# Kernel tuning notes

Measured on AMD Instinct MI355X. Metric: run time of the kernel, lower is better.

Reference implementation:

```python
import jax, jax.numpy as jnp
import numpy as np

B, L, C, R = 8192, 49, 512, 128  # L = 7*7 hardcoded in module
H = W = 7


def _conv2d(x, w, b, pad):
    # x: (B, Cin, H, W), w: (Cout, Cin, k, k)
    y = jax.lax.conv_general_dilated(
        x, w, window_strides=(1, 1), padding=[(pad, pad), (pad, pad)],
        dimension_numbers=("NCHW", "OIHW", "NCHW"))
    return y + b[None, :, None, None]


def _star_relu(x, scale, bias):
    r = jnp.maximum(x, 0.0)
    return scale * (r * r) + bias


def setup_inputs() -> dict:
    key = jax.random.key(0)
    ks = jax.random.split(key, 12)
    s = 0.05
    return {
        "x": jax.random.normal(ks[0], (B, L, C), jnp.float32),
        "g_reduce_w": jax.random.normal(ks[1], (R, C), jnp.float32) * s,
        "l_reduce_w": jax.random.normal(ks[2], (R, C), jnp.float32) * s,
        "conv3_w": jax.random.normal(ks[3], (R // 2, R // 2, 3, 3), jnp.float32) * s,
        "conv3_b": jax.random.normal(ks[4], (R // 2,), jnp.float32) * s,
        "conv5_w": jax.random.normal(ks[5], (R - R // 2, R - R // 2, 5, 5), jnp.float32) * s,
        "conv5_b": jax.random.normal(ks[6], (R - R // 2,), jnp.float32) * s,
        "channel_w": jax.random.normal(ks[7], (C, R), jnp.float32) * s,
        "channel_b": jax.random.normal(ks[8], (C,), jnp.float32) * s,
        "spatial_w": jax.random.normal(ks[9], (1, 3 * R), jnp.float32) * s,
        "spatial_b": jax.random.normal(ks[10], (1,), jnp.float32) * s,
        "star_scale": jnp.ones((1,), jnp.float32),
        "star_bias": jnp.zeros((1,), jnp.float32),
    }


def reference(x, g_reduce_w, l_reduce_w, conv3_w, conv3_b, conv5_w, conv5_b,
              channel_w, channel_b, spatial_w, spatial_b, star_scale, star_bias):
    # x: (B, L, C) with L = 49 (7x7)
    # Global dual pooling over spatial (== over L)
    x_max = jnp.max(x, axis=1)   # (B, C)
    x_avg = jnp.mean(x, axis=1)  # (B, C)
    # g_reduce 1x1 conv (no bias) + StarReLU
    g1 = _star_relu(x_max @ g_reduce_w.T, star_scale, star_bias)  # (B, R)
    g2 = _star_relu(x_avg @ g_reduce_w.T, star_scale, star_bias)  # (B, R)
    # Local branch: 1x1 reduce -> HybConv2d (split 3x3 / 5x5) -> StarReLU
    x_img = x.transpose(0, 2, 1).reshape(B, C, H, W)
    x_l = jnp.einsum("bchw,rc->brhw", x_img, l_reduce_w)  # (B, R, 7, 7)
    xl1, xl2 = x_l[:, :R // 2], x_l[:, R // 2:]
    y1 = _conv2d(xl1, conv3_w, conv3_b, pad=1)
    y2 = _conv2d(xl2, conv5_w, conv5_b, pad=2)
    x_l = _star_relu(jnp.concatenate([y1, y2], axis=1), star_scale, star_bias)
    x_l = x_l.reshape(B, R, L).transpose(0, 2, 1)  # (B, L, R)
    # Channel gate: Linear(R->C) applied to each pooled branch, summed
    c_aggr = jax.nn.sigmoid((g1 @ channel_w.T + channel_b)
                            + (g2 @ channel_w.T + channel_b))  # (B, C)
    # Spatial gate: concat [x_l, g1 broadcast, g2 broadcast] -> Linear(3R->1)
    g1b = jnp.broadcast_to(g1[:, None, :], (B, L, R))
    g2b = jnp.broadcast_to(g2[:, None, :], (B, L, R))
    s_cat = jnp.concatenate([x_l, g1b, g2b], axis=-1)  # (B, L, 3R)
    s_aggr = jax.nn.sigmoid(jnp.einsum("blk,ok->blo", s_cat, spatial_w) + spatial_b)  # (B, L, 1)
    aggr = c_aggr[:, None, :] * s_aggr  # (B, L, C)
    return x * aggr
```

## Files before the change

kernel.cpp:

```cpp
#include <hip/hip_runtime.h>
#include <math.h>

#define B_ 8192
#define L_ 49
#define C_ 512
#define R_ 128

typedef short   bf16x8 __attribute__((ext_vector_type(8)));
typedef unsigned short u16x8 __attribute__((ext_vector_type(8)));
typedef float   f32x4  __attribute__((ext_vector_type(4)));

#define WS_LWF   0
#define WS_WB3F  65536
#define WS_WB5F  102400
#define WS_GWF   204800
#define WS_CWF   270336

#define SM_G     0
#define SM_CA    1024
#define SM_SPW   3072
#define SM_SP    5120
#define SM_GDOT  5376
#define SM_XB    0
#define SM_XLB   50176
#define SM_MAXB  50176
#define SM_SUMF  54272
#define SM_GA    62976
#define SM_TOT   65024

__device__ __forceinline__ float bf2f(unsigned short u) {
    union { float f; unsigned int i; } v; v.i = ((unsigned int)u) << 16; return v.f;
}
__device__ __forceinline__ unsigned short f2bf(float f) {
    union { float f; unsigned int i; } v; v.f = f;
    unsigned int r = v.i + 0x7fffu + ((v.i >> 16) & 1u);
    return (unsigned short)(r >> 16);
}
__device__ __forceinline__ float star_relu(float x, float sc, float bi) {
    float r = fmaxf(x, 0.f);
    return sc * r * r + bi;
}
__device__ __forceinline__ float sigmoidf_(float x) {
    return 1.f / (1.f + __expf(-x));
}

__global__ void cvt_weights(const float* __restrict__ lw, const float* __restrict__ w3,
                            const float* __restrict__ w5, const float* __restrict__ gw,
                            const float* __restrict__ cw, unsigned short* __restrict__ ws)
{
    int t = blockIdx.x * blockDim.x + threadIdx.x;
    int stride = gridDim.x * blockDim.x;
    for (int i = t; i < 65536; i += stride) {
        int j = i & 7, lane = (i >> 3) & 63, ks = (i >> 9) & 15, nt = i >> 13;
        int n = nt * 16 + (lane & 15);
        int k = ks * 32 + (lane >> 4) * 8 + j;
        ws[WS_LWF + i] = f2bf(lw[n * 512 + k]);
        ws[WS_GWF + i] = f2bf(gw[n * 512 + k]);
    }
    for (int i = t; i < 65536; i += stride) {
        int j = i & 7, c = (i >> 3) & 511, r8 = i >> 12;
        ws[WS_CWF + i] = f2bf(cw[c * 128 + r8 * 8 + j]);
    }
    for (int i = t; i < 36864; i += stride) {
        int j = i & 7, lane = (i >> 3) & 63, ks = (i >> 9) & 1, f = (i >> 10) & 3, tap = i >> 12;
        int oc = f * 16 + (lane & 15);
        int ic = ks * 32 + (lane >> 4) * 8 + j;
        ws[WS_WB3F + i] = f2bf(w3[(oc * 64 + ic) * 9 + tap]);
    }
    for (int i = t; i < 102400; i += stride) {
        int j = i & 7, lane = (i >> 3) & 63, ks = (i >> 9) & 1, f = (i >> 10) & 3, tap = i >> 12;
        int oc = f * 16 + (lane & 15);
        int ic = ks * 32 + (lane >> 4) * 8 + j;
        ws[WS_WB5F + i] = f2bf(w5[(oc * 64 + ic) * 25 + tap]);
    }
}

template <int NTAP, int KD, int PAD, int COLBASE>
__device__ __forceinline__ void conv_mfma(const unsigned short* __restrict__ s_xlb,
                                          const unsigned short* __restrict__ wtbf,
                                          int m16, int kg, int ln, int f, f32x4 C[4])
{
    int lp_[4], i_[4], j_[4];
    #pragma unroll
    for (int mf = 0; mf < 4; ++mf) {
        lp_[mf] = mf * 16 + m16;
        i_[mf] = lp_[mf] / 7;
        j_[mf] = lp_[mf] % 7;
    }
    bf16x8 cur0 = *(const bf16x8*)(wtbf + ((0 * 4 + f) * 2 + 0) * 512 + ln * 8);
    bf16x8 cur1 = *(const bf16x8*)(wtbf + ((0 * 4 + f) * 2 + 1) * 512 + ln * 8);
    #pragma unroll
    for (int tap = 0; tap < NTAP; ++tap) {
        bf16x8 nxt0 = cur0, nxt1 = cur1;
        if (tap + 1 < NTAP) {
            nxt0 = *(const bf16x8*)(wtbf + (((tap + 1) * 4 + f) * 2 + 0) * 512 + ln * 8);
            nxt1 = *(const bf16x8*)(wtbf + (((tap + 1) * 4 + f) * 2 + 1) * 512 + ln * 8);
        }
        const int dy = tap / KD - PAD, dx = tap % KD - PAD;
        int lc[4];
        #pragma unroll
        for (int mf = 0; mf < 4; ++mf) {
            int ii = i_[mf] + dy, jj = j_[mf] + dx;
            bool v = (lp_[mf] < 49) & (ii >= 0) & (ii < 7) & (jj >= 0) & (jj < 7);
            lc[mf] = v ? (ii * 7 + jj) : 49;
        }
        #pragma unroll
        for (int mf = 0; mf < 4; ++mf) {
            int chunk0 = ((COLBASE >> 3) + kg) ^ (lc[mf] & 7);
            bf16x8 a = *(const bf16x8*)&s_xlb[lc[mf] * 128 + chunk0 * 8];
            C[mf] = __builtin_amdgcn_mfma_f32_16x16x32_bf16(a, cur0, C[mf], 0, 0, 0);
        }
        #pragma unroll
        for (int mf = 0; mf < 4; ++mf) {
            int chunk1 = ((COLBASE >> 3) + 4 + kg) ^ (lc[mf] & 7);
            bf16x8 a = *(const bf16x8*)&s_xlb[lc[mf] * 128 + chunk1 * 8];
            C[mf] = __builtin_amdgcn_mfma_f32_16x16x32_bf16(a, cur1, C[mf], 0, 0, 0);
        }
        cur0 = nxt0; cur1 = nxt1;
    }
}

__global__ __launch_bounds__(512, 4)
void mafn_fused(const float* __restrict__ x,
                const float* __restrict__ b3, const float* __restrict__ b5,
                const float* __restrict__ cb, const float* __restrict__ sw,
                const float* __restrict__ sb, const float* __restrict__ ssc,
                const float* __restrict__ sbi,
                const unsigned short* __restrict__ ws,
                float* __restrict__ out)
{
    __shared__ __align__(16) unsigned char smem[SM_TOT];
    unsigned short* s_xb   = (unsigned short*)(smem + SM_XB);
    unsigned short* s_xlb  = (unsigned short*)(smem + SM_XLB);
    unsigned short* s_maxb = (unsigned short*)(smem + SM_MAXB);
    float*          s_sumf = (float*)(smem + SM_SUMF);
    unsigned short* s_ga   = (unsigned short*)(smem + SM_GA);
    float*          s_g    = (float*)(smem + SM_G);
    float*          s_ca   = (float*)(smem + SM_CA);
    float*          s_spw  = (float*)(smem + SM_SPW);
    float*          s_sp   = (float*)(smem + SM_SP);
    float*          s_gdot = (float*)(smem + SM_GDOT);

    const int b = blockIdx.x, t = threadIdx.x;
    const int wv = t >> 6, ln = t & 63;
    const int m16 = ln & 15, kg = ln >> 4;
    const float scale = ssc[0], sbias = sbi[0];

    const unsigned short* lwf  = ws + WS_LWF;
    const unsigned short* wb3f = ws + WS_WB3F;
    const unsigned short* wb5f = ws + WS_WB5F;
    const unsigned short* gwf  = ws + WS_GWF;
    const unsigned short* cwf  = ws + WS_CWF;

    f32x4 accA[4];
    f32x4 accG;
    {
        const f32x4 z = {0.f, 0.f, 0.f, 0.f};
        #pragma unroll
        for (int mf = 0; mf < 4; ++mf) accA[mf] = z;
        accG = z;
    }

    {
        const float4* x4 = (const float4*)(x + (size_t)b * (L_ * C_));
        const int c4 = t & 127, rg = t >> 7;
        const int l0 = rg * 12;
        const int nl = (rg < 3) ? 12 : 13;
        float4 mx = {-3.4e38f, -3.4e38f, -3.4e38f, -3.4e38f};
        float4 sm = {0.f, 0.f, 0.f, 0.f};
        for (int li = 0; li < nl; ++li) {
            int l = l0 + li;
            float4 v = x4[l * 128 + c4];
            mx.x = fmaxf(mx.x, v.x); mx.y = fmaxf(mx.y, v.y);
            mx.z = fmaxf(mx.z, v.z); mx.w = fmaxf(mx.w, v.w);
            sm.x += v.x; sm.y += v.y; sm.z += v.z; sm.w += v.w;
            ushort4 p;
            p.x = f2bf(v.x); p.y = f2bf(v.y); p.z = f2bf(v.z); p.w = f2bf(v.w);
            int chunk = (c4 >> 1) ^ (l & 7);
            *(ushort4*)&s_xb[l * 512 + chunk * 8 + (c4 & 1) * 4] = p;
        }
        ushort4 pm;
        pm.x = f2bf(mx.x); pm.y = f2bf(mx.y); pm.z = f2bf(mx.z); pm.w = f2bf(mx.w);
        *(ushort4*)&s_maxb[rg * 512 + c4 * 4] = pm;
        *(float4*)&s_sumf[rg * 512 + c4 * 4] = sm;
    }
    __syncthreads();

    {
        int c = t;
        float m = bf2f(s_maxb[c]);
        #pragma unroll
        for (int i = 1; i < 4; ++i) m = fmaxf(m, bf2f(s_maxb[i * 512 + c]));
        float s = 0.f;
        #pragma unroll
        for (int i = 0; i < 4; ++i) s += s_sumf[i * 512 + c];
        s_ga[c] = f2bf(m);
        s_ga[512 + c] = f2bf(s * (1.f / 49.f));
    }
    __syncthreads();

    {
        int rowA[4];
        #pragma unroll
        for (int mf = 0; mf < 4; ++mf) rowA[mf] = min(mf * 16 + m16, 48);

        bf16x8 bb0 = *(const bf16x8*)(lwf + (wv * 16 + 0) * 512 + ln * 8);
        bf16x8 bb1 = *(const bf16x8*)(lwf + (wv * 16 + 1) * 512 + ln * 8);
        #pragma unroll
        for (int ks = 0; ks < 16; ++ks) {
            bf16x8 bn = bb1;
            if (ks + 2 < 16)
                bn = *(const bf16x8*)(lwf + (wv * 16 + ks + 2) * 512 + ln * 8);
            #pragma unroll
            for (int mf = 0; mf < 4; ++mf) {
                int chunk = (ks * 4 + kg) ^ (rowA[mf] & 7);
                bf16x8 a = *(const bf16x8*)&s_xb[rowA[mf] * 512 + chunk * 8];
                accA[mf] = __builtin_amdgcn_mfma_f32_16x16x32_bf16(a, bb0, accA[mf], 0, 0, 0);
            }
            bb0 = bb1; bb1 = bn;
        }

        bf16x8 gb0 = *(const bf16x8*)(gwf + (wv * 16 + 0) * 512 + ln * 8);
        bf16x8 gb1 = *(const bf16x8*)(gwf + (wv * 16 + 1) * 512 + ln * 8);
        const bf16x8 zz = {0,0,0,0,0,0,0,0};
        #pragma unroll
        for (int ks = 0; ks < 16; ++ks) {
            bf16x8 gn = gb1;
            if (ks + 2 < 16)
                gn = *(const bf16x8*)(gwf + (wv * 16 + ks + 2) * 512 + ln * 8);
            bf16x8 a = (m16 < 2) ? *(const bf16x8*)&s_ga[m16 * 512 + ks * 32 + kg * 8] : zz;
            accG = __builtin_amdgcn_mfma_f32_16x16x32_bf16(a, gb0, accG, 0, 0, 0);
            gb0 = gb1; gb1 = gn;
        }
    }
    __syncthreads();

    {
        if (t < 64) ((unsigned int*)(s_xlb + 49 * 128))[t] = 0;
        const int n = wv * 16 + m16;
        #pragma unroll
        for (int mf = 0; mf < 4; ++mf) {
            #pragma unroll
            for (int rg = 0; rg < 4; ++rg) {
                int lp = mf * 16 + kg * 4 + rg;
                if (lp < 49) {
                    int idx = lp * 128 + ((((n >> 3) ^ (lp & 7)) << 3) + (n & 7));
                    s_xlb[idx] = f2bf(accA[mf][rg]);
                }
            }
        }
        if (kg == 0) {
            s_g[n]       = star_relu(accG[0], scale, sbias);
            s_g[128 + n] = star_relu(accG[1], scale, sbias);
        }
    }
    __syncthreads();

    const int f_ = wv & 3;
    const int oc_ = f_ * 16 + m16;
    {
        f32x4 C[4];
        const f32x4 z = {0.f, 0.f, 0.f, 0.f};
        #pragma unroll
        for (int mf = 0; mf < 4; ++mf) C[mf] = z;

        if (wv < 4) {
            conv_mfma<25, 5, 2, 64>(s_xlb, wb5f, m16, kg, ln, f_, C);
        } else {
            conv_mfma< 9, 3, 1,  0>(s_xlb, wb3f, m16, kg, ln, f_, C);
            const int idx = t - 256;
            #pragma unroll
            for (int half = 0; half < 2; ++half) {
                int c = idx + half * 256;
                float a0 = 0.f, a1 = 0.f;
                #pragma unroll 4
                for (int r8 = 0; r8 < 16; ++r8) {
                    u16x8 w = *(const u16x8*)(cwf + r8 * 4096 + c * 8);
                    float p = 0.f;
                    #pragma unroll
                    for (int k = 0; k < 8; ++k)
                        p += bf2f(w[k]) * (s_g[r8 * 8 + k] + s_g[128 + r8 * 8 + k]);
                    if (r8 & 1) a1 += p; else a0 += p;
                }
                s_ca[c] = sigmoidf_(a0 + a1 + 2.f * cb[c]);
            }
            if (wv == 7) {
                float p = s_g[ln] * sw[128 + ln] + s_g[128 + ln] * sw[256 + ln]
                        + s_g[ln + 64] * sw[128 + ln + 64] + s_g[128 + ln + 64] * sw[256 + ln + 64];
                #pragma unroll
                for (int off = 32; off > 0; off >>= 1) p += __shfl_xor(p, off);
                if (ln == 0) s_gdot[0] = p;
            }
        }

        const bool is5 = (wv < 4);
        const int ch = is5 ? 64 + oc_ : oc_;
        const float bias = is5 ? b5[oc_] : b3[oc_];
        const float sww = sw[ch];
        #pragma unroll
        for (int mf = 0; mf < 4; ++mf) {
            #pragma unroll
            for (int rg = 0; rg < 4; ++rg) {
                int lp = mf * 16 + kg * 4 + rg;
                float v = (lp < 49) ? star_relu(C[mf][rg] + bias, scale, sbias) * sww : 0.f;
                v += __shfl_xor(v, 1);
                v += __shfl_xor(v, 2);
                v += __shfl_xor(v, 4);
                v += __shfl_xor(v, 8);
                if (m16 == 0 && lp < 49) s_spw[wv * 64 + lp] = v;
            }
        }
    }
    __syncthreads();

    if (t < 49) {
        float s = s_gdot[0] + sb[0];
        #pragma unroll
        for (int w = 0; w < 8; ++w) s += s_spw[w * 64 + t];
        s_sp[t] = sigmoidf_(s);
    }
    __syncthreads();

    {
        const float4* x4 = (const float4*)(x + (size_t)b * (L_ * C_));
        float4* o4 = (float4*)(out + (size_t)b * (L_ * C_));
        const int c4 = t & 127;
        const float4 cv = *(const float4*)&s_ca[c4 * 4];
        for (int i = t; i < 49 * 128; i += 512) {
            int l = i >> 7;
            float4 xv = x4[i];
            float g = s_sp[l];
            float4 ov;
            ov.x = xv.x * cv.x * g;
            ov.y = xv.y * cv.y * g;
            ov.z = xv.z * cv.z * g;
            ov.w = xv.w * cv.w * g;
            o4[i] = ov;
        }
    }
}

extern "C" void kernel_launch(void* const* d_in, const int* in_sizes, int n_in,
                              void* d_out, int out_size, void* d_ws, size_t ws_size,
                              hipStream_t stream) {
    (void)in_sizes; (void)n_in; (void)ws_size; (void)out_size;
    const float* x    = (const float*)d_in[0];
    const float* g_w  = (const float*)d_in[1];
    const float* l_w  = (const float*)d_in[2];
    const float* w3   = (const float*)d_in[3];
    const float* b3   = (const float*)d_in[4];
    const float* w5   = (const float*)d_in[5];
    const float* b5   = (const float*)d_in[6];
    const float* cw   = (const float*)d_in[7];
    const float* cb   = (const float*)d_in[8];
    const float* sw   = (const float*)d_in[9];
    const float* sb   = (const float*)d_in[10];
    const float* ssc  = (const float*)d_in[11];
    const float* sbi  = (const float*)d_in[12];
    float* outp = (float*)d_out;
    unsigned short* ws = (unsigned short*)d_ws;

    cvt_weights<<<dim3(512), dim3(256), 0, stream>>>(l_w, w3, w5, g_w, cw, ws);
    mafn_fused<<<dim3(B_), dim3(512), 0, stream>>>(
        x, b3, b5, cb, sw, sb, ssc, sbi, ws, outp);
}
```

Measured before the change: 602.2 us.

## Drop fourth conv MFMA row tile and compute last pixel with scalar FMAs

The conv MFMA loop now covers only three 16-row tiles (pixels 0-47). Pixel 48 is computed separately on the 3x3 waves with scalar FP32 dot products over raw weights, then reduced by shuffles and an LDS atomic. The goal is to cut about a quarter of conv MFMA work and A-fragment LDS reads. Bf16 packing also moves to the v_cvt_pk_bf16_f32 instruction. In exchange, the 3x3 waves carry extra scalar work and uncoalesced global weight reads, which may lengthen the critical path.

```diff
diff --git a/kernel.cpp b/kernel.cpp
--- a/kernel.cpp
+++ b/kernel.cpp
@@ -35,6 +35,11 @@
     union { float f; unsigned int i; } v; v.f = f;
     unsigned int r = v.i + 0x7fffu + ((v.i >> 16) & 1u);
     return (unsigned short)(r >> 16);
+}
+__device__ __forceinline__ unsigned int pkbf(float a, float b) {
+    unsigned int r;
+    asm("v_cvt_pk_bf16_f32 %0, %1, %2" : "=v"(r) : "v"(a), "v"(b));
+    return r;
 }
 __device__ __forceinline__ float star_relu(float x, float sc, float bi) {
     float r = fmaxf(x, 0.f);
@@ -78,11 +83,11 @@
 template <int NTAP, int KD, int PAD, int COLBASE>
 __device__ __forceinline__ void conv_mfma(const unsigned short* __restrict__ s_xlb,
                                           const unsigned short* __restrict__ wtbf,
-                                          int m16, int kg, int ln, int f, f32x4 C[4])
+                                          int m16, int kg, int ln, int f, f32x4 C[3])
 {
-    int lp_[4], i_[4], j_[4];
+    int lp_[3], i_[3], j_[3];
     #pragma unroll
-    for (int mf = 0; mf < 4; ++mf) {
+    for (int mf = 0; mf < 3; ++mf) {
         lp_[mf] = mf * 16 + m16;
         i_[mf] = lp_[mf] / 7;
         j_[mf] = lp_[mf] % 7;
@@ -97,21 +102,21 @@
             nxt1 = *(const bf16x8*)(wtbf + (((tap + 1) * 4 + f) * 2 + 1) * 512 + ln * 8);
         }
         const int dy = tap / KD - PAD, dx = tap % KD - PAD;
-        int lc[4];
-        #pragma unroll
-        for (int mf = 0; mf < 4; ++mf) {
+        int lc[3];
+        #pragma unroll
+        for (int mf = 0; mf < 3; ++mf) {
             int ii = i_[mf] + dy, jj = j_[mf] + dx;
-            bool v = (lp_[mf] < 49) & (ii >= 0) & (ii < 7) & (jj >= 0) & (jj < 7);
+            bool v = (ii >= 0) & (ii < 7) & (jj >= 0) & (jj < 7);
             lc[mf] = v ? (ii * 7 + jj) : 49;
         }
         #pragma unroll
-        for (int mf = 0; mf < 4; ++mf) {
+        for (int mf = 0; mf < 3; ++mf) {
             int chunk0 = ((COLBASE >> 3) + kg) ^ (lc[mf] & 7);
             bf16x8 a = *(const bf16x8*)&s_xlb[lc[mf] * 128 + chunk0 * 8];
             C[mf] = __builtin_amdgcn_mfma_f32_16x16x32_bf16(a, cur0, C[mf], 0, 0, 0);
         }
         #pragma unroll
-        for (int mf = 0; mf < 4; ++mf) {
+        for (int mf = 0; mf < 3; ++mf) {
             int chunk1 = ((COLBASE >> 3) + 4 + kg) ^ (lc[mf] & 7);
             bf16x8 a = *(const bf16x8*)&s_xlb[lc[mf] * 128 + chunk1 * 8];
             C[mf] = __builtin_amdgcn_mfma_f32_16x16x32_bf16(a, cur1, C[mf], 0, 0, 0);
@@ -126,6 +131,7 @@
                 const float* __restrict__ cb, const float* __restrict__ sw,
                 const float* __restrict__ sb, const float* __restrict__ ssc,
                 const float* __restrict__ sbi,
+                const float* __restrict__ w3raw, const float* __restrict__ w5raw,
                 const unsigned short* __restrict__ ws,
                 float* __restrict__ out)
 {
@@ -174,14 +180,12 @@
             mx.x = fmaxf(mx.x, v.x); mx.y = fmaxf(mx.y, v.y);
             mx.z = fmaxf(mx.z, v.z); mx.w = fmaxf(mx.w, v.w);
             sm.x += v.x; sm.y += v.y; sm.z += v.z; sm.w += v.w;
-            ushort4 p;
-            p.x = f2bf(v.x); p.y = f2bf(v.y); p.z = f2bf(v.z); p.w = f2bf(v.w);
+            uint2 p; p.x = pkbf(v.x, v.y); p.y = pkbf(v.z, v.w);
             int chunk = (c4 >> 1) ^ (l & 7);
-            *(ushort4*)&s_xb[l * 512 + chunk * 8 + (c4 & 1) * 4] = p;
-        }
-        ushort4 pm;
-        pm.x = f2bf(mx.x); pm.y = f2bf(mx.y); pm.z = f2bf(mx.z); pm.w = f2bf(mx.w);
-        *(ushort4*)&s_maxb[rg * 512 + c4 * 4] = pm;
+            *(uint2*)&s_xb[l * 512 + chunk * 8 + (c4 & 1) * 4] = p;
+        }
+        uint2 pm; pm.x = pkbf(mx.x, mx.y); pm.y = pkbf(mx.z, mx.w);
+        *(uint2*)&s_maxb[rg * 512 + c4 * 4] = pm;
         *(float4*)&s_sumf[rg * 512 + c4 * 4] = sm;
     }
     __syncthreads();
@@ -237,15 +241,22 @@
 
     {
         if (t < 64) ((unsigned int*)(s_xlb + 49 * 128))[t] = 0;
+        if (t < 8)  s_spw[t * 64 + 48] = 0.f;
+        if (t == 8) s_gdot[1] = 0.f;
         const int n = wv * 16 + m16;
         #pragma unroll
         for (int mf = 0; mf < 4; ++mf) {
             #pragma unroll
-            for (int rg = 0; rg < 4; ++rg) {
-                int lp = mf * 16 + kg * 4 + rg;
-                if (lp < 49) {
-                    int idx = lp * 128 + ((((n >> 3) ^ (lp & 7)) << 3) + (n & 7));
-                    s_xlb[idx] = f2bf(accA[mf][rg]);
+            for (int rp = 0; rp < 2; ++rp) {
+                unsigned int u = pkbf(accA[mf][rp * 2], accA[mf][rp * 2 + 1]);
+                int lp0 = mf * 16 + kg * 4 + rp * 2;
+                if (lp0 < 49) {
+                    int idx = lp0 * 128 + ((((n >> 3) ^ (lp0 & 7)) << 3) + (n & 7));
+                    s_xlb[idx] = (unsigned short)u;
+                }
+                if (lp0 + 1 < 49) {
+                    int idx = (lp0 + 1) * 128 + ((((n >> 3) ^ ((lp0 + 1) & 7)) << 3) + (n & 7));
+                    s_xlb[idx] = (unsigned short)(u >> 16);
                 }
             }
         }
@@ -259,10 +270,10 @@
     const int f_ = wv & 3;
     const int oc_ = f_ * 16 + m16;
     {
-        f32x4 C[4];
+        f32x4 C[3];
         const f32x4 z = {0.f, 0.f, 0.f, 0.f};
         #pragma unroll
-        for (int mf = 0; mf < 4; ++mf) C[mf] = z;
+        for (int mf = 0; mf < 3; ++mf) C[mf] = z;
 
         if (wv < 4) {
             conv_mfma<25, 5, 2, 64>(s_xlb, wb5f, m16, kg, ln, f_, C);
@@ -284,6 +295,40 @@
                 }
                 s_ca[c] = sigmoidf_(a0 + a1 + 2.f * cb[c]);
             }
+            {
+                const int ch = idx >> 2;
+                const int q  = idx & 3;
+                float pre5 = 0.f, pre3 = 0.f;
+                #pragma unroll
+                for (int ii = 4; ii <= 6; ++ii) {
+                    #pragma unroll
+                    for (int jj = 4; jj <= 6; ++jj) {
+                        const int lp = ii * 7 + jj;
+                        const int tap5 = (ii - 4) * 5 + (jj - 4);
+                        for (int i = 0; i < 16; ++i) {
+                            int ic = q * 16 + i;
+                            int n5 = 64 + ic;
+                            float xv = bf2f(s_xlb[lp * 128 + (((n5 >> 3) ^ (lp & 7)) << 3) + (n5 & 7)]);
+                            pre5 += xv * w5raw[(ch * 64 + ic) * 25 + tap5];
+                        }
+                        if (ii >= 5 && jj >= 5) {
+                            const int tap3 = (ii - 5) * 3 + (jj - 5);
+                            for (int i = 0; i < 16; ++i) {
+                                int ic = q * 16 + i;
+                                float xv = bf2f(s_xlb[lp * 128 + (((ic >> 3) ^ (lp & 7)) << 3) + (ic & 7)]);
+                                pre3 += xv * w3raw[(ch * 64 + ic) * 9 + tap3];
+                            }
+                        }
+                    }
+                }
+                pre5 += __shfl_xor(pre5, 1); pre5 += __shfl_xor(pre5, 2);
+                pre3 += __shfl_xor(pre3, 1); pre3 += __shfl_xor(pre3, 2);
+                float v = star_relu(pre5 + b5[ch], scale, sbias) * sw[64 + ch]
+                        + star_relu(pre3 + b3[ch], scale, sbias) * sw[ch];
+                v += __shfl_xor(v, 4); v += __shfl_xor(v, 8);
+                v += __shfl_xor(v, 16); v += __shfl_xor(v, 32);
+                if (ln == 0) atomicAdd(&s_gdot[1], v);
+            }
             if (wv == 7) {
                 float p = s_g[ln] * sw[128 + ln] + s_g[128 + ln] * sw[256 + ln]
                         + s_g[ln + 64] * sw[128 + ln + 64] + s_g[128 + ln + 64] * sw[256 + ln + 64];
@@ -298,16 +343,16 @@
         const float bias = is5 ? b5[oc_] : b3[oc_];
         const float sww = sw[ch];
         #pragma unroll
-        for (int mf = 0; mf < 4; ++mf) {
+        for (int mf = 0; mf < 3; ++mf) {
             #pragma unroll
             for (int rg = 0; rg < 4; ++rg) {
                 int lp = mf * 16 + kg * 4 + rg;
-                float v = (lp < 49) ? star_relu(C[mf][rg] + bias, scale, sbias) * sww : 0.f;
+                float v = star_relu(C[mf][rg] + bias, scale, sbias) * sww;
                 v += __shfl_xor(v, 1);
                 v += __shfl_xor(v, 2);
                 v += __shfl_xor(v, 4);
                 v += __shfl_xor(v, 8);
-                if (m16 == 0 && lp < 49) s_spw[wv * 64 + lp] = v;
+                if (m16 == 0) s_spw[wv * 64 + lp] = v;
             }
         }
     }
@@ -317,6 +362,7 @@
         float s = s_gdot[0] + sb[0];
         #pragma unroll
         for (int w = 0; w < 8; ++w) s += s_spw[w * 64 + t];
+        if (t == 48) s += s_gdot[1];
         s_sp[t] = sigmoidf_(s);
     }
     __syncthreads();
@@ -362,5 +408,5 @@
 
     cvt_weights<<<dim3(512), dim3(256), 0, stream>>>(l_w, w3, w5, g_w, cw, ws);
     mafn_fused<<<dim3(B_), dim3(512), 0, stream>>>(
-        x, b3, b5, cb, sw, sb, ssc, sbi, ws, outp);
-}
+        x, b3, b5, cb, sw, sb, ssc, sbi, w3, w5, ws, outp);
+}
```

Result: slower. 1.140 ms (+89.3%).
